# Kernel optimization log

Measured on AMD Instinct MI355X. Metric: run time of the kernel, lower is better.

## Reference

```python
import jax, jax.numpy as jnp
import numpy as np

N0, E0 = 50000, 200000
N1 = E0 // 2          # 100000 path nodes (pairs of graph0 edges)
E1 = 400000
ATOM_F, BOND_F, IN_F, H = 128, 128, 64, 2


def _egat(src, dst, n_nodes, nfeats, efeats, W_ni, W_nj, W_fij, W_node, b_node, attn, bias, out_n, out_e):
    # edge feature: f_ni[src] + f_nj[dst] + fc_fij(efeats) + bias
    f = (nfeats @ W_ni)[src] + (nfeats @ W_nj)[dst] + efeats @ W_fij + bias
    f = jax.nn.leaky_relu(f).reshape(-1, H, out_e)          # [E, H, out_e]
    e = jnp.sum(f * attn, axis=-1)                          # [E, H] attention logits
    # edge softmax over incoming edges of each dst node
    emax = jax.ops.segment_max(e, dst, num_segments=n_nodes)
    ee = jnp.exp(e - emax[dst])
    a = ee / jax.ops.segment_sum(ee, dst, num_segments=n_nodes)[dst]   # [E, H]
    h = (nfeats @ W_node + b_node).reshape(-1, H, out_n)    # [N, H, out_n]
    h_out = jax.ops.segment_sum(h[src] * a[..., None], dst, num_segments=n_nodes)
    return h_out, f


def setup_inputs() -> dict:
    key = jax.random.key(0)
    it = iter(jax.random.split(key, 64))
    def nrm(shape, s=0.1):
        return jax.random.normal(next(it), shape, jnp.float32) * s
    inp = {
        'node_feats': nrm((N0, ATOM_F), 1.0),
        'edge_feats': nrm((E0, BOND_F), 1.0),
        'node_path': nrm((N1, BOND_F), 1.0),
        'edge_path': nrm((E1, IN_F), 1.0),
    }
    def egat_params(pre, in_n, in_e, out_n, out_e):
        inp[pre + '_ni'] = nrm((in_n, out_e * H))
        inp[pre + '_nj'] = nrm((in_n, out_e * H))
        inp[pre + '_fij'] = nrm((in_e, out_e * H))
        inp[pre + '_node'] = nrm((in_n, out_n * H))
        inp[pre + '_bnode'] = nrm((out_n * H,))
        inp[pre + '_attn'] = nrm((1, H, out_e))
        inp[pre + '_bias'] = nrm((out_e * H,))
    egat_params('L1', ATOM_F, BOND_F, ATOM_F, BOND_F)
    egat_params('L2a', BOND_F, IN_F, BOND_F, IN_F)
    egat_params('L2b', BOND_F, IN_F, BOND_F, IN_F)
    egat_params('L3', ATOM_F, BOND_F, ATOM_F, BOND_F)
    inp['lin1_W'] = nrm((2 * BOND_F, BOND_F))
    inp['lin1_b'] = nrm((BOND_F,))
    # graphs: arange prefix on dst guarantees in-degree >= 1 for every node
    inp['src0'] = jax.random.randint(next(it), (E0,), 0, N0)
    inp['dst0'] = jnp.concatenate([jnp.arange(N0), jax.random.randint(next(it), (E0 - N0,), 0, N0)])
    inp['src1'] = jax.random.randint(next(it), (E1,), 0, N1)
    inp['dst1'] = jnp.concatenate([jnp.arange(N1), jax.random.randint(next(it), (E1 - N1,), 0, N1)])
    return inp


def reference(node_feats, edge_feats, node_path, edge_path,
              L1_ni, L1_nj, L1_fij, L1_node, L1_bnode, L1_attn, L1_bias,
              L2a_ni, L2a_nj, L2a_fij, L2a_node, L2a_bnode, L2a_attn, L2a_bias,
              L2b_ni, L2b_nj, L2b_fij, L2b_node, L2b_bnode, L2b_attn, L2b_bias,
              L3_ni, L3_nj, L3_fij, L3_node, L3_bnode, L3_attn, L3_bias,
              lin1_W, lin1_b, src0, dst0, src1, dst1):
    ini_y3 = node_path
    # ---- stage 1: EGAT on atom graph ----
    h, f = _egat(src0, dst0, N0, node_feats, edge_feats,
                 L1_ni, L1_nj, L1_fij, L1_node, L1_bnode, L1_attn, L1_bias, ATOM_F, BOND_F)
    nf = h.sum(axis=1)            # [N0, ATOM_F]
    ef = f.sum(axis=1)            # [E0, BOND_F]
    # ---- edge-pair -> path-node lift ----
    x11 = jnp.concatenate([ef[0::2], ef[1::2]], axis=1)     # [N1, 2*BOND_F]
    node_path = x11 @ lin1_W + lin1_b + ini_y3              # [N1, BOND_F]
    # ---- stage 2: EGAT layers on path graph ----
    for p in ((L2a_ni, L2a_nj, L2a_fij, L2a_node, L2a_bnode, L2a_attn, L2a_bias),
              (L2b_ni, L2b_nj, L2b_fij, L2b_node, L2b_bnode, L2b_attn, L2b_bias)):
        h, f = _egat(src1, dst1, N1, node_path, edge_path, *p, BOND_F, IN_F)
        node_path = h.sum(axis=1)  # [N1, BOND_F]
        edge_path = f.sum(axis=1)  # [E1, IN_F]
    # ---- path-node -> edge feats for atom graph (each row repeated twice) ----
    ef2 = jnp.repeat(node_path, 2, axis=0)                  # [E0, BOND_F]
    # ---- stage 3: EGAT on atom graph again ----
    h, f = _egat(src0, dst0, N0, nf, ef2,
                 L3_ni, L3_nj, L3_fij, L3_node, L3_bnode, L3_attn, L3_bias, ATOM_F, BOND_F)
    nf = h.sum(axis=1)
    ef2 = f.sum(axis=1)
    return (nf, ef2, node_path, edge_path)
```

## Files before the change

kernel.cpp:

```cpp
#include <hip/hip_runtime.h>

#define CN0 50000
#define CE0 200000
#define CN1 100000
#define CE1 400000

typedef __attribute__((ext_vector_type(8))) _Float16 half8;
typedef __attribute__((ext_vector_type(4))) _Float16 half4;
typedef __attribute__((ext_vector_type(4))) float floatx4;

__global__ void fill_k(float* __restrict__ p, float v, int n) {
    int i = blockIdx.x * 256 + threadIdx.x;
    if (i < n) p[i] = v;
}

struct WtDesc { const float* W; _Float16* T; int KM; int mshift; int K; };
struct WtArgs { WtDesc d[17]; };

__global__ __launch_bounds__(256) void wcvt_k(WtArgs a) {
    WtDesc w = a.d[blockIdx.y];
    const int M1 = (1 << w.mshift) - 1;
    for (int i = blockIdx.x * 256 + threadIdx.x; i < w.KM; i += 256 * gridDim.x) {
        int k = i >> w.mshift, m = i & M1;
        w.T[(long)m * w.K + k] = (_Float16)w.W[i];
    }
}

__global__ void hist2_k(const int* __restrict__ dst0, const int* __restrict__ dst1,
                        int* __restrict__ deg0, int* __restrict__ deg1) {
    int i = blockIdx.x * 256 + threadIdx.x;
    if (i < CE0) atomicAdd(&deg0[dst0[i]], 1);
    if (i < CE1) atomicAdd(&deg1[dst1[i]], 1);
}

__global__ __launch_bounds__(256) void scanA_k(const int* __restrict__ deg, int N,
                                               int* __restrict__ off, int* __restrict__ bsum) {
    __shared__ int s[256];
    int t = threadIdx.x, i = blockIdx.x * 256 + t;
    int v = (i < N) ? deg[i] : 0;
    s[t] = v; __syncthreads();
    #pragma unroll
    for (int d = 1; d < 256; d <<= 1) {
        int x = (t >= d) ? s[t - d] : 0;
        __syncthreads(); s[t] += x; __syncthreads();
    }
    if (i < N) off[i] = s[t] - v;
    if (t == 255) bsum[blockIdx.x] = s[255];
}

__global__ __launch_bounds__(256) void scanB_k(int* __restrict__ bsum0, int nb0,
                                               int* __restrict__ bsum1, int nb1) {
    int* bs = blockIdx.x ? bsum1 : bsum0;
    int nb  = blockIdx.x ? nb1 : nb0;
    __shared__ int s[256];
    __shared__ int tot, carry;
    int t = threadIdx.x;
    if (t == 0) carry = 0;
    __syncthreads();
    for (int base = 0; base < nb; base += 256) {
        int i = base + t;
        int v = (i < nb) ? bs[i] : 0;
        s[t] = v; __syncthreads();
        #pragma unroll
        for (int d = 1; d < 256; d <<= 1) {
            int x = (t >= d) ? s[t - d] : 0;
            __syncthreads(); s[t] += x; __syncthreads();
        }
        if (i < nb) bs[i] = s[t] - v + carry;
        if (t == 255) tot = s[255];
        __syncthreads();
        if (t == 0) carry += tot;
        __syncthreads();
    }
}

__global__ void scanC_k(int* __restrict__ off, const int* __restrict__ bsum, int N, int E) {
    int i = blockIdx.x * 256 + threadIdx.x;
    if (i < N) off[i] += bsum[i >> 8];
    if (i == 0) off[N] = E;
}

__global__ void csrfill2_k(const int* __restrict__ src0, const int* __restrict__ dst0,
                           const int* __restrict__ off0, int* __restrict__ cur0,
                           int* __restrict__ csrc0, int* __restrict__ pos0,
                           const int* __restrict__ src1, const int* __restrict__ dst1,
                           const int* __restrict__ off1, int* __restrict__ cur1,
                           int* __restrict__ csrc1, int* __restrict__ pos1) {
    int i = blockIdx.x * 256 + threadIdx.x;
    if (i < CE0) {
        int d = dst0[i];
        int slot = off0[d] + atomicAdd(&cur0[d], 1);
        csrc0[slot] = src0[i];
        pos0[i] = slot;
    }
    if (i < CE1) {
        int d = dst1[i];
        int slot = off1[d] + atomicAdd(&cur1[d], 1);
        csrc1[slot] = src1[i];
        pos1[i] = slot;
    }
}

__global__ __launch_bounds__(256) void gemm_k(
        const float* __restrict__ X, const _Float16* __restrict__ Wt,
        const float* __restrict__ bias, const float* __restrict__ add,
        float* __restrict__ Y, int N, int K, int M) {
    __shared__ _Float16 As[128 * 64];
    char* asb = (char*)As;
    const int tid = threadIdx.x;
    const int lane = tid & 63;
    const int wid = tid >> 6;
    const int wr = wid >> 1, wc = wid & 1;
    const int bm = blockIdx.y * 128;
    const int bn = blockIdx.x * 128;
    const int l15 = lane & 15, lk = lane >> 4;

    floatx4 acc[4][4] = {};

    for (int k0 = 0; k0 < K; k0 += 64) {
        #pragma unroll
        for (int i = 0; i < 8; ++i) {
            int f = tid + i * 256;
            int r = f >> 4, kq = f & 15;
            int gr = bm + r;
            float4 v = make_float4(0.f, 0.f, 0.f, 0.f);
            if (gr < N) v = *(const float4*)&X[(long)gr * K + k0 + kq * 4];
            half4 hv = { (_Float16)v.x, (_Float16)v.y, (_Float16)v.z, (_Float16)v.w };
            int byte = (r * 128 + kq * 8) ^ ((r & 7) << 4);
            *(half4*)(asb + byte) = hv;
        }
        half8 bf[2][4];
        #pragma unroll
        for (int kk = 0; kk < 2; ++kk)
            #pragma unroll
            for (int ct = 0; ct < 4; ++ct) {
                int col = bn + wc * 64 + ct * 16 + l15;
                bf[kk][ct] = *(const half8*)&Wt[(long)col * K + k0 + kk * 32 + lk * 8];
            }
        __syncthreads();
        #pragma unroll
        for (int kk = 0; kk < 2; ++kk) {
            half8 af[4];
            #pragma unroll
            for (int rt = 0; rt < 4; ++rt) {
                int row = wr * 64 + rt * 16 + l15;
                int byte = (row * 128 + (kk * 32 + lk * 8) * 2) ^ ((row & 7) << 4);
                af[rt] = *(const half8*)(asb + byte);
            }
            #pragma unroll
            for (int rt = 0; rt < 4; ++rt)
                #pragma unroll
                for (int ct = 0; ct < 4; ++ct)
                    acc[rt][ct] = __builtin_amdgcn_mfma_f32_16x16x32_f16(
                        af[rt], bf[kk][ct], acc[rt][ct], 0, 0, 0);
        }
        __syncthreads();
    }
    #pragma unroll
    for (int ct = 0; ct < 4; ++ct) {
        int col = bn + wc * 64 + ct * 16 + l15;
        float bv = bias ? bias[col] : 0.f;
        #pragma unroll
        for (int rt = 0; rt < 4; ++rt) {
            #pragma unroll
            for (int r = 0; r < 4; ++r) {
                int row = bm + wr * 64 + rt * 16 + lk * 4 + r;
                if (row < N) {
                    float v = acc[rt][ct][r] + bv;
                    long off = (long)row * M + col;
                    if (add) v += add[off];
                    Y[off] = v;
                }
            }
        }
    }
}

__global__ __launch_bounds__(256) void edge_k(
        const float* __restrict__ FNi, const float* __restrict__ FNj,
        const float* __restrict__ FEb, const float* __restrict__ attn,
        const int* __restrict__ src, const int* __restrict__ dst,
        const int* __restrict__ pos,
        int E, int out_e, int fe_shift,
        float* __restrict__ ef_out, float* __restrict__ clog) {
    int e = blockIdx.x * 4 + (threadIdx.x >> 6);
    int lane = threadIdx.x & 63;
    if (e >= E) return;
    int s = src[e], d = dst[e];
    long fi = (long)s * (2 * out_e);
    long fj = (long)d * (2 * out_e);
    long fe = (long)(e >> fe_shift) * (2 * out_e);
    float l0 = 0.f, l1 = 0.f;
    for (int c = lane; c < out_e; c += 64) {
        float f0 = FNi[fi + c] + FNj[fj + c] + FEb[fe + c];
        f0 = f0 > 0.f ? f0 : 0.01f * f0;
        float f1 = FNi[fi + out_e + c] + FNj[fj + out_e + c] + FEb[fe + out_e + c];
        f1 = f1 > 0.f ? f1 : 0.01f * f1;
        l0 += f0 * attn[c];
        l1 += f1 * attn[out_e + c];
        ef_out[(long)e * out_e + c] = f0 + f1;
    }
    #pragma unroll
    for (int off = 32; off > 0; off >>= 1) {
        l0 += __shfl_down(l0, off);
        l1 += __shfl_down(l1, off);
    }
    if (lane == 0) {
        int p = pos[e];
        float2 lv = { l0, l1 };
        *(float2*)&clog[2 * p] = lv;
    }
}

__global__ __launch_bounds__(256) void aggregate_k(
        const float* __restrict__ Hn, const float* __restrict__ clog,
        const int* __restrict__ off, const int* __restrict__ csrc,
        int N, float* __restrict__ out) {
    int n = blockIdx.x * 4 + (threadIdx.x >> 6);
    int lane = threadIdx.x & 63;
    if (n >= N) return;
    int i0 = off[n], i1 = off[n + 1];
    float m0 = -3.0e38f, m1 = -3.0e38f;
    for (int i = i0; i < i1; ++i) {
        float2 l = *(const float2*)&clog[2 * i];
        m0 = fmaxf(m0, l.x);
        m1 = fmaxf(m1, l.y);
    }
    float s0 = 0.f, s1 = 0.f;
    float2 accA = make_float2(0.f, 0.f), accB = make_float2(0.f, 0.f);
    for (int i = i0; i < i1; ++i) {
        float2 l = *(const float2*)&clog[2 * i];
        float w0 = __expf(l.x - m0);
        float w1 = __expf(l.y - m1);
        s0 += w0; s1 += w1;
        const float* h = Hn + (long)csrc[i] * 256;
        float2 h0 = *(const float2*)&h[2 * lane];
        float2 h1 = *(const float2*)&h[128 + 2 * lane];
        accA.x += w0 * h0.x; accA.y += w0 * h0.y;
        accB.x += w1 * h1.x; accB.y += w1 * h1.y;
    }
    float r0 = 1.f / s0, r1 = 1.f / s1;
    float2 o;
    o.x = accA.x * r0 + accB.x * r1;
    o.y = accA.y * r0 + accB.y * r1;
    *(float2*)&out[(long)n * 128 + 2 * lane] = o;
}

extern "C" void kernel_launch(void* const* d_in, const int* in_sizes, int n_in,
                              void* d_out, int out_size, void* d_ws, size_t ws_size,
                              hipStream_t stream) {
    const float* node_feats   = (const float*)d_in[0];
    const float* edge_feats   = (const float*)d_in[1];
    const float* node_path_in = (const float*)d_in[2];
    const float* edge_path_in = (const float*)d_in[3];
    const float* lin1_b = (const float*)d_in[33];
    const int* src0 = (const int*)d_in[34];
    const int* dst0 = (const int*)d_in[35];
    const int* src1 = (const int*)d_in[36];
    const int* dst1 = (const int*)d_in[37];

    float* out  = (float*)d_out;
    float* seg0 = out;
    float* seg1 = out + 6400000;
    float* seg2 = out + 32000000;
    float* seg3 = out + 44800000;

    float* ws     = (float*)d_ws;
    float* FNi    = ws;
    float* FNj    = FNi + 12800000;
    float* Hn     = FNj + 12800000;
    float* FE     = Hn  + 25600000;
    float* EF     = FE  + 51200000;
    float* np2    = EF  + 25600000;
    float* logits = np2 + 12800000;
    _Float16* WT  = (_Float16*)(logits + 800000);
    int* ib    = (int*)(WT + 442368);
    int* off0  = ib;
    int* csrc0 = off0 + 50001;
    int* off1  = csrc0 + 200000;
    int* csrc1 = off1 + 100001;
    int* pos0  = csrc1 + 400000;
    int* pos1  = pos0 + 200000;
    int* deg0  = pos1 + 400000;
    int* cur0  = deg0 + 50000;
    int* deg1  = cur0 + 50000;
    int* cur1  = deg1 + 100000;
    int* bsum0 = cur1 + 100000;
    int* bsum1 = bsum0 + 196;

    const int nb0 = (CN0 + 255) / 256;
    const int nb1 = (CN1 + 255) / 256;

    static const int wi_din[17]  = {4,5,6,7, 11,12,13,14, 18,19,20,21, 25,26,27,28, 32};
    static const int wi_K[17]    = {128,128,128,128, 128,128,64,128, 128,128,64,128, 128,128,128,128, 256};
    static const int wi_M[17]    = {256,256,256,256, 128,128,128,256, 128,128,128,256, 256,256,256,256, 128};
    _Float16* wt[17];
    {
        _Float16* p = WT;
        for (int i = 0; i < 17; ++i) { wt[i] = p; p += (size_t)wi_K[i] * wi_M[i]; }
    }
    {
        WtArgs a;
        for (int i = 0; i < 17; ++i) {
            a.d[i].W = (const float*)d_in[wi_din[i]];
            a.d[i].T = wt[i];
            a.d[i].KM = wi_K[i] * wi_M[i];
            a.d[i].mshift = (wi_M[i] == 256) ? 8 : 7;
            a.d[i].K = wi_K[i];
        }
        wcvt_k<<<dim3(4, 17), 256, 0, stream>>>(a);
    }

    fill_k<<<(300000 + 255) / 256, 256, 0, stream>>>((float*)deg0, 0.f, 300000);
    hist2_k<<<(CE1 + 255) / 256, 256, 0, stream>>>(dst0, dst1, deg0, deg1);
    scanA_k<<<nb0, 256, 0, stream>>>(deg0, CN0, off0, bsum0);
    scanA_k<<<nb1, 256, 0, stream>>>(deg1, CN1, off1, bsum1);
    scanB_k<<<2, 256, 0, stream>>>(bsum0, nb0, bsum1, nb1);
    scanC_k<<<nb0, 256, 0, stream>>>(off0, bsum0, CN0, CE0);
    scanC_k<<<nb1, 256, 0, stream>>>(off1, bsum1, CN1, CE1);
    csrfill2_k<<<(CE1 + 255) / 256, 256, 0, stream>>>(src0, dst0, off0, cur0, csrc0, pos0,
                                                      src1, dst1, off1, cur1, csrc1, pos1);

    auto gemm = [&](const float* X, const _Float16* Wt, const float* b, const float* add,
                    float* Y, int N, int K, int M) {
        dim3 g(M / 128, (N + 127) / 128);
        gemm_k<<<g, 256, 0, stream>>>(X, Wt, b, add, Y, N, K, M);
    };
    auto egat = [&](const float* nfeats, int N, int in_n,
                    const float* efeats, int fij_rows, int in_e,
                    int out_e, int fe_shift, int base, int wb,
                    const int* src, const int* dst, int E,
                    const int* off, const int* csrc, const int* pos,
                    float* ef_out, float* h_out) {
        const float* bnode = (const float*)d_in[base + 4];
        const float* attn  = (const float*)d_in[base + 5];
        const float* bias  = (const float*)d_in[base + 6];
        gemm(nfeats, wt[wb + 0], nullptr, nullptr, FNi, N, in_n, 2 * out_e);
        gemm(nfeats, wt[wb + 1], nullptr, nullptr, FNj, N, in_n, 2 * out_e);
        gemm(nfeats, wt[wb + 3], bnode,   nullptr, Hn,  N, in_n, 256);
        gemm(efeats, wt[wb + 2], bias,    nullptr, FE,  fij_rows, in_e, 2 * out_e);
        edge_k<<<(E + 3) / 4, 256, 0, stream>>>(FNi, FNj, FE, attn, src, dst, pos,
                                                E, out_e, fe_shift, ef_out, logits);
        aggregate_k<<<(N + 3) / 4, 256, 0, stream>>>(Hn, logits, off, csrc, N, h_out);
    };

    egat(node_feats, CN0, 128, edge_feats, CE0, 128, 128, 0, 4, 0,
         src0, dst0, CE0, off0, csrc0, pos0, seg1, seg0);

    gemm(seg1, wt[16], lin1_b, node_path_in, seg2, CN1, 256, 128);

    egat(seg2, CN1, 128, edge_path_in, CE1, 64, 64, 0, 11, 4,
         src1, dst1, CE1, off1, csrc1, pos1, EF, np2);

    egat(np2, CN1, 128, EF, CE1, 64, 64, 0, 18, 8,
         src1, dst1, CE1, off1, csrc1, pos1, seg3, seg2);

    egat(seg0, CN0, 128, seg2, CN1, 128, 128, 1, 25, 12,
         src0, dst0, CE0, off0, csrc0, pos0, seg1, seg0);
}
```

Before: 2.483 ms.

## Fuse node GEMMs into one fp16-output GEMM with interleaved head layout

The three node-side GEMMs (W_ni, W_nj, W_node) are merged into one GEMM over a concatenated, column-permuted weight so the input is read once and a single launch is issued. GEMM outputs are stored as fp16 with the two heads interleaved, so edge_k and aggregate_k can load half2 pairs and move half as many bytes per gather. The node bias is moved into the aggregate epilogue, which is valid because the softmax weights sum to one. In exchange, intermediate features lose precision by being stored in fp16.

```diff
diff --git a/kernel.cpp b/kernel.cpp
--- a/kernel.cpp
+++ b/kernel.cpp
@@ -7,6 +7,7 @@
 
 typedef __attribute__((ext_vector_type(8))) _Float16 half8;
 typedef __attribute__((ext_vector_type(4))) _Float16 half4;
+typedef __attribute__((ext_vector_type(2))) _Float16 half2h;
 typedef __attribute__((ext_vector_type(4))) float floatx4;
 
 __global__ void fill_k(float* __restrict__ p, float v, int n) {
@@ -14,7 +15,7 @@
     if (i < n) p[i] = v;
 }
 
-struct WtDesc { const float* W; _Float16* T; int KM; int mshift; int K; };
+struct WtDesc { const float* W; _Float16* T; int KM; int mshift; int K; int oesh; };
 struct WtArgs { WtDesc d[17]; };
 
 __global__ __launch_bounds__(256) void wcvt_k(WtArgs a) {
@@ -22,7 +23,21 @@
     const int M1 = (1 << w.mshift) - 1;
     for (int i = blockIdx.x * 256 + threadIdx.x; i < w.KM; i += 256 * gridDim.x) {
         int k = i >> w.mshift, m = i & M1;
-        w.T[(long)m * w.K + k] = (_Float16)w.W[i];
+        int m2 = w.oesh ? (((m & ((1 << w.oesh) - 1)) << 1) | (m >> w.oesh)) : m;
+        w.T[(long)m2 * w.K + k] = (_Float16)w.W[i];
+    }
+}
+
+struct BpDesc { const float* b; float* o; int oe; };
+struct BpArgs { BpDesc d[4]; };
+
+__global__ __launch_bounds__(256) void bperm_k(BpArgs a) {
+    BpDesc d = a.d[blockIdx.x];
+    int m = threadIdx.x;
+    if (m < 2 * d.oe) {
+        int h = (m >= d.oe) ? 1 : 0;
+        int c = m - h * d.oe;
+        d.o[2 * c + h] = d.b[m];
     }
 }
 
@@ -101,10 +116,11 @@
     }
 }
 
-__global__ __launch_bounds__(256) void gemm_k(
+template <typename TO>
+__global__ __launch_bounds__(256) void gemm_t(
         const float* __restrict__ X, const _Float16* __restrict__ Wt,
         const float* __restrict__ bias, const float* __restrict__ add,
-        float* __restrict__ Y, int N, int K, int M) {
+        TO* __restrict__ Y, int N, int K, int M) {
     __shared__ _Float16 As[128 * 64];
     char* asb = (char*)As;
     const int tid = threadIdx.x;
@@ -167,9 +183,9 @@
                 int row = bm + wr * 64 + rt * 16 + lk * 4 + r;
                 if (row < N) {
                     float v = acc[rt][ct][r] + bv;
-                    long off = (long)row * M + col;
-                    if (add) v += add[off];
-                    Y[off] = v;
+                    long o = (long)row * M + col;
+                    if (add) v += add[o];
+                    Y[o] = (TO)v;
                 }
             }
         }
@@ -177,28 +193,31 @@
 }
 
 __global__ __launch_bounds__(256) void edge_k(
-        const float* __restrict__ FNi, const float* __restrict__ FNj,
-        const float* __restrict__ FEb, const float* __restrict__ attn,
+        const _Float16* __restrict__ FN, const _Float16* __restrict__ FE,
+        const float* __restrict__ attn,
         const int* __restrict__ src, const int* __restrict__ dst,
         const int* __restrict__ pos,
-        int E, int out_e, int fe_shift,
+        int E, int oe, int fe_shift, int nstride,
         float* __restrict__ ef_out, float* __restrict__ clog) {
     int e = blockIdx.x * 4 + (threadIdx.x >> 6);
     int lane = threadIdx.x & 63;
     if (e >= E) return;
     int s = src[e], d = dst[e];
-    long fi = (long)s * (2 * out_e);
-    long fj = (long)d * (2 * out_e);
-    long fe = (long)(e >> fe_shift) * (2 * out_e);
+    long fi = (long)s * nstride;
+    long fj = (long)d * nstride + 2 * oe;
+    long fe = (long)(e >> fe_shift) * (2 * oe);
     float l0 = 0.f, l1 = 0.f;
-    for (int c = lane; c < out_e; c += 64) {
-        float f0 = FNi[fi + c] + FNj[fj + c] + FEb[fe + c];
+    for (int c = lane; c < oe; c += 64) {
+        half2h a = *(const half2h*)&FN[fi + 2 * c];
+        half2h b = *(const half2h*)&FN[fj + 2 * c];
+        half2h g = *(const half2h*)&FE[fe + 2 * c];
+        float f0 = (float)a.x + (float)b.x + (float)g.x;
         f0 = f0 > 0.f ? f0 : 0.01f * f0;
-        float f1 = FNi[fi + out_e + c] + FNj[fj + out_e + c] + FEb[fe + out_e + c];
+        float f1 = (float)a.y + (float)b.y + (float)g.y;
         f1 = f1 > 0.f ? f1 : 0.01f * f1;
         l0 += f0 * attn[c];
-        l1 += f1 * attn[out_e + c];
-        ef_out[(long)e * out_e + c] = f0 + f1;
+        l1 += f1 * attn[oe + c];
+        ef_out[(long)e * oe + c] = f0 + f1;
     }
     #pragma unroll
     for (int off = 32; off > 0; off >>= 1) {
@@ -213,9 +232,9 @@
 }
 
 __global__ __launch_bounds__(256) void aggregate_k(
-        const float* __restrict__ Hn, const float* __restrict__ clog,
-        const int* __restrict__ off, const int* __restrict__ csrc,
-        int N, float* __restrict__ out) {
+        const _Float16* __restrict__ Hn, int stride, const float* __restrict__ bnode,
+        const float* __restrict__ clog, const int* __restrict__ off,
+        const int* __restrict__ csrc, int N, float* __restrict__ out) {
     int n = blockIdx.x * 4 + (threadIdx.x >> 6);
     int lane = threadIdx.x & 63;
     if (n >= N) return;
@@ -233,16 +252,16 @@
         float w0 = __expf(l.x - m0);
         float w1 = __expf(l.y - m1);
         s0 += w0; s1 += w1;
-        const float* h = Hn + (long)csrc[i] * 256;
-        float2 h0 = *(const float2*)&h[2 * lane];
-        float2 h1 = *(const float2*)&h[128 + 2 * lane];
-        accA.x += w0 * h0.x; accA.y += w0 * h0.y;
-        accB.x += w1 * h1.x; accB.y += w1 * h1.y;
+        const _Float16* h = Hn + (long)csrc[i] * stride;
+        half2h h0 = *(const half2h*)&h[2 * lane];
+        half2h h1 = *(const half2h*)&h[128 + 2 * lane];
+        accA.x += w0 * (float)h0.x; accA.y += w0 * (float)h0.y;
+        accB.x += w1 * (float)h1.x; accB.y += w1 * (float)h1.y;
     }
     float r0 = 1.f / s0, r1 = 1.f / s1;
     float2 o;
-    o.x = accA.x * r0 + accB.x * r1;
-    o.y = accA.y * r0 + accB.y * r1;
+    o.x = accA.x * r0 + accB.x * r1 + bnode[2 * lane]     + bnode[128 + 2 * lane];
+    o.y = accA.y * r0 + accB.y * r1 + bnode[2 * lane + 1] + bnode[128 + 2 * lane + 1];
     *(float2*)&out[(long)n * 128 + 2 * lane] = o;
 }
 
@@ -265,15 +284,14 @@
     float* seg2 = out + 32000000;
     float* seg3 = out + 44800000;
 
-    float* ws     = (float*)d_ws;
-    float* FNi    = ws;
-    float* FNj    = FNi + 12800000;
-    float* Hn     = FNj + 12800000;
-    float* FE     = Hn  + 25600000;
-    float* EF     = FE  + 51200000;
-    float* np2    = EF  + 25600000;
-    float* logits = np2 + 12800000;
-    _Float16* WT  = (_Float16*)(logits + 800000);
+    float* ws      = (float*)d_ws;
+    _Float16* FN   = (_Float16*)ws;
+    _Float16* FE16 = FN + 51200000;
+    float* EF   = (float*)(FE16 + 51200000);
+    float* np2  = EF + 25600000;
+    float* clog = np2 + 12800000;
+    float* biasI = clog + 800000;
+    _Float16* WT = (_Float16*)(biasI + 1024);
     int* ib    = (int*)(WT + 442368);
     int* off0  = ib;
     int* csrc0 = off0 + 50001;
@@ -291,24 +309,41 @@
     const int nb0 = (CN0 + 255) / 256;
     const int nb1 = (CN1 + 255) / 256;
 
-    static const int wi_din[17]  = {4,5,6,7, 11,12,13,14, 18,19,20,21, 25,26,27,28, 32};
-    static const int wi_K[17]    = {128,128,128,128, 128,128,64,128, 128,128,64,128, 128,128,128,128, 256};
-    static const int wi_M[17]    = {256,256,256,256, 128,128,128,256, 128,128,128,256, 256,256,256,256, 128};
-    _Float16* wt[17];
+    static const int wi_din[17]  = {4,5,7,6, 11,12,14,13, 18,19,21,20, 25,26,28,27, 32};
+    static const int wi_M[17]    = {256,256,256,256, 128,128,256,128, 128,128,256,128, 256,256,256,256, 128};
+    static const int wi_K[17]    = {128,128,128,128, 128,128,128,64, 128,128,128,64, 128,128,128,128, 256};
+    static const int wi_oesh[17] = {7,7,0,7, 6,6,0,6, 6,6,0,6, 7,7,0,7, 0};
+    _Float16* wtp[17];
     {
         _Float16* p = WT;
-        for (int i = 0; i < 17; ++i) { wt[i] = p; p += (size_t)wi_K[i] * wi_M[i]; }
-    }
+        for (int i = 0; i < 17; ++i) { wtp[i] = p; p += (size_t)wi_M[i] * wi_K[i]; }
+    }
+    _Float16* nodeW[4] = { wtp[0], wtp[4], wtp[8],  wtp[12] };
+    _Float16* fijW[4]  = { wtp[3], wtp[7], wtp[11], wtp[15] };
+    _Float16* lin1t    = wtp[16];
     {
         WtArgs a;
         for (int i = 0; i < 17; ++i) {
             a.d[i].W = (const float*)d_in[wi_din[i]];
-            a.d[i].T = wt[i];
-            a.d[i].KM = wi_K[i] * wi_M[i];
+            a.d[i].T = wtp[i];
+            a.d[i].KM = wi_M[i] * wi_K[i];
             a.d[i].mshift = (wi_M[i] == 256) ? 8 : 7;
             a.d[i].K = wi_K[i];
+            a.d[i].oesh = wi_oesh[i];
         }
         wcvt_k<<<dim3(4, 17), 256, 0, stream>>>(a);
+    }
+    float* biasL[4] = { biasI, biasI + 256, biasI + 384, biasI + 512 };
+    {
+        BpArgs b;
+        static const int bdin[4] = {10, 17, 24, 31};
+        static const int boe[4]  = {128, 64, 64, 128};
+        for (int i = 0; i < 4; ++i) {
+            b.d[i].b = (const float*)d_in[bdin[i]];
+            b.d[i].o = biasL[i];
+            b.d[i].oe = boe[i];
+        }
+        bperm_k<<<4, 256, 0, stream>>>(b);
     }
 
     fill_k<<<(300000 + 255) / 256, 256, 0, stream>>>((float*)deg0, 0.f, 300000);
@@ -321,40 +356,46 @@
     csrfill2_k<<<(CE1 + 255) / 256, 256, 0, stream>>>(src0, dst0, off0, cur0, csrc0, pos0,
                                                       src1, dst1, off1, cur1, csrc1, pos1);
 
-    auto gemm = [&](const float* X, const _Float16* Wt, const float* b, const float* add,
-                    float* Y, int N, int K, int M) {
-        dim3 g(M / 128, (N + 127) / 128);
-        gemm_k<<<g, 256, 0, stream>>>(X, Wt, b, add, Y, N, K, M);
-    };
     auto egat = [&](const float* nfeats, int N, int in_n,
                     const float* efeats, int fij_rows, int in_e,
-                    int out_e, int fe_shift, int base, int wb,
+                    int oe, int fe_shift, int base, int L,
                     const int* src, const int* dst, int E,
                     const int* off, const int* csrc, const int* pos,
                     float* ef_out, float* h_out) {
         const float* bnode = (const float*)d_in[base + 4];
         const float* attn  = (const float*)d_in[base + 5];
-        const float* bias  = (const float*)d_in[base + 6];
-        gemm(nfeats, wt[wb + 0], nullptr, nullptr, FNi, N, in_n, 2 * out_e);
-        gemm(nfeats, wt[wb + 1], nullptr, nullptr, FNj, N, in_n, 2 * out_e);
-        gemm(nfeats, wt[wb + 3], bnode,   nullptr, Hn,  N, in_n, 256);
-        gemm(efeats, wt[wb + 2], bias,    nullptr, FE,  fij_rows, in_e, 2 * out_e);
-        edge_k<<<(E + 3) / 4, 256, 0, stream>>>(FNi, FNj, FE, attn, src, dst, pos,
-                                                E, out_e, fe_shift, ef_out, logits);
-        aggregate_k<<<(N + 3) / 4, 256, 0, stream>>>(Hn, logits, off, csrc, N, h_out);
+        const int Mtot = 4 * oe + 256;
+        {
+            dim3 g(Mtot / 128, (N + 127) / 128);
+            gemm_t<_Float16><<<g, 256, 0, stream>>>(nfeats, nodeW[L], nullptr, nullptr,
+                                                    FN, N, in_n, Mtot);
+        }
+        {
+            dim3 g((2 * oe) / 128, (fij_rows + 127) / 128);
+            gemm_t<_Float16><<<g, 256, 0, stream>>>(efeats, fijW[L], biasL[L], nullptr,
+                                                    FE16, fij_rows, in_e, 2 * oe);
+        }
+        edge_k<<<(E + 3) / 4, 256, 0, stream>>>(FN, FE16, attn, src, dst, pos,
+                                                E, oe, fe_shift, Mtot, ef_out, clog);
+        aggregate_k<<<(N + 3) / 4, 256, 0, stream>>>(FN + 4 * oe, Mtot, bnode,
+                                                     clog, off, csrc, N, h_out);
     };
 
     egat(node_feats, CN0, 128, edge_feats, CE0, 128, 128, 0, 4, 0,
          src0, dst0, CE0, off0, csrc0, pos0, seg1, seg0);
 
-    gemm(seg1, wt[16], lin1_b, node_path_in, seg2, CN1, 256, 128);
-
-    egat(seg2, CN1, 128, edge_path_in, CE1, 64, 64, 0, 11, 4,
+    {
+        dim3 g(1, (CN1 + 127) / 128);
+        gemm_t<float><<<g, 256, 0, stream>>>(seg1, lin1t, lin1_b, node_path_in,
+                                             seg2, CN1, 256, 128);
+    }
+
+    egat(seg2, CN1, 128, edge_path_in, CE1, 64, 64, 0, 11, 1,
          src1, dst1, CE1, off1, csrc1, pos1, EF, np2);
 
-    egat(np2, CN1, 128, EF, CE1, 64, 64, 0, 18, 8,
+    egat(np2, CN1, 128, EF, CE1, 64, 64, 0, 18, 2,
          src1, dst1, CE1, off1, csrc1, pos1, seg3, seg2);
 
-    egat(seg0, CN0, 128, seg2, CN1, 128, 128, 1, 25, 12,
+    egat(seg0, CN0, 128, seg2, CN1, 128, 128, 1, 25, 3,
          src0, dst0, CE0, off0, csrc0, pos0, seg1, seg0);
 }
```

Result: faster. 2.181 ms (-12.2%).
